# Performance work log

Hardware: AMD Instinct MI355X
Metric: run time of the kernel (lower is better)

The kernel has to match this reference:

```python
import jax, jax.numpy as jnp
import numpy as np

E, D, H = 8, 512, 2048  # num_experts, features, features*mlp_ratio
B, S = 4, 512


def _lecun(key, shape):
    fan_in = shape[-2] if len(shape) >= 2 else shape[0]
    return jax.random.normal(key, shape, dtype=jnp.float32) / jnp.sqrt(jnp.float32(fan_in))


def setup_inputs() -> dict:
    key = jax.random.key(0)
    ks = jax.random.split(key, 8)
    return {
        'x_real': jax.random.normal(ks[0], (B, S, D), dtype=jnp.float32),
        'x_imag': jax.random.normal(ks[1], (B, S, D), dtype=jnp.float32),
        # gating Dense over concat([amp, phase]) -> in_features = 2*D
        'gate_W': _lecun(ks[2], (2 * D, E)),
        'gate_b': jnp.zeros((E,), jnp.float32),
        # per-expert ComplexLinear 1: D -> H
        'W1r': _lecun(ks[3], (E, D, H)),
        'W1i': _lecun(ks[4], (E, D, H)),
        'b1r': jnp.zeros((E, H), jnp.float32),
        'b1i': jnp.zeros((E, H), jnp.float32),
        # per-expert ComplexModReLU bias
        'mod_b': jnp.zeros((E, H), jnp.float32),
        # per-expert ComplexLinear 2: H -> D
        'W2r': _lecun(ks[5], (E, H, D)),
        'W2i': _lecun(ks[6], (E, H, D)),
        'b2r': jnp.zeros((E, D), jnp.float32),
        'b2i': jnp.zeros((E, D), jnp.float32),
    }


def reference(x_real, x_imag, gate_W, gate_b, W1r, W1i, b1r, b1i, mod_b, W2r, W2i, b2r, b2i):
    eps = 1e-10
    # --- gating: scores over [|z|, angle(z)] ---
    amp = jnp.sqrt(x_real ** 2 + x_imag ** 2)            # |z|, [B,S,D]
    phase = jnp.arctan2(x_imag, x_real)                  # angle(z)
    routing_input = jnp.concatenate([amp, phase], axis=-1)  # [B,S,2D]
    scores = routing_input @ gate_W + gate_b             # [B,S,E]
    probs = jax.nn.softmax(scores, axis=-1)
    idx = jnp.argmax(probs, axis=-1)                     # [B,S] top-1 expert

    # --- all experts dense (faithful to reference): complex linear 1 ---
    # (Wr + iWi)(xr + ixi) : hr = xr Wr - xi Wi ; hi = xr Wi + xi Wr
    h_r = (jnp.einsum('bsd,edh->ebsh', x_real, W1r)
           - jnp.einsum('bsd,edh->ebsh', x_imag, W1i)) + b1r[:, None, None, :]
    h_i = (jnp.einsum('bsd,edh->ebsh', x_real, W1i)
           + jnp.einsum('bsd,edh->ebsh', x_imag, W1r)) + b1i[:, None, None, :]

    # --- ComplexModReLU: relu(|z|+b) * z / (|z|+eps), |z| = sqrt(r^2+i^2+eps) ---
    a = jnp.sqrt(h_r ** 2 + h_i ** 2 + eps)              # [E,B,S,H]
    scale = jax.nn.relu(a + mod_b[:, None, None, :]) / (a + eps)
    h_r = h_r * scale
    h_i = h_i * scale

    # --- complex linear 2 ---
    o_r = (jnp.einsum('ebsh,ehd->ebsd', h_r, W2r)
           - jnp.einsum('ebsh,ehd->ebsd', h_i, W2i)) + b2r[:, None, None, :]
    o_i = (jnp.einsum('ebsh,ehd->ebsd', h_r, W2i)
           + jnp.einsum('ebsh,ehd->ebsd', h_i, W2r)) + b2i[:, None, None, :]

    # --- mask + weight (top-1): out = sum_e out_e * probs[...,e] * (argmax==e) ---
    e_ids = jnp.arange(probs.shape[-1])
    w = jnp.transpose(probs, (2, 0, 1)) * (idx[None, :, :] == e_ids[:, None, None])  # [E,B,S]
    out_r = jnp.einsum('ebs,ebsd->bsd', w, o_r)
    out_i = jnp.einsum('ebs,ebsd->bsd', w, o_i)
    return (out_r, out_i)
```

## Files before the change

### kernel.cpp

```cpp
#include <hip/hip_runtime.h>
#include <math.h>

#define NE 8
#define ND 512
#define NH 2048
#define NT 2048

typedef __attribute__((ext_vector_type(8))) short short8;
typedef __attribute__((ext_vector_type(4))) float f32x4;

#define GLL(g, d) __builtin_amdgcn_global_load_lds( \
    (const __attribute__((address_space(1))) void*)(g), \
    (__attribute__((address_space(3))) void*)(d), 16, 0, 0)

__device__ __forceinline__ unsigned short f2bf(float x) {
    unsigned int u = __builtin_bit_cast(unsigned int, x);
    u += 0x7FFFu + ((u >> 16) & 1u);
    return (unsigned short)(u >> 16);
}

__device__ __forceinline__ short8 neg8(short8 v) {
    int4 u = __builtin_bit_cast(int4, v);
    u.x ^= 0x80008000; u.y ^= 0x80008000; u.z ^= 0x80008000; u.w ^= 0x80008000;
    return __builtin_bit_cast(short8, u);
}

__device__ __forceinline__ short8 lds8(const unsigned short* p) {
    return *(const short8*)p;
}

__global__ __launch_bounds__(256) void gate_kernel(
    const float* __restrict__ xr, const float* __restrict__ xi,
    const float* __restrict__ gW, const float* __restrict__ gb,
    float* __restrict__ gate_w,
    int* __restrict__ counts, int* __restrict__ tok_list)
{
    int t = blockIdx.x;
    int tid = threadIdx.x;
    const float* xrt = xr + (size_t)t * ND;
    const float* xit = xi + (size_t)t * ND;

    float acc[NE] = {0,0,0,0,0,0,0,0};
    for (int r = tid; r < 2 * ND; r += 256) {
        int d = r & (ND - 1);
        float a = xrt[d], b = xit[d];
        float v = (r < ND) ? sqrtf(a * a + b * b) : atan2f(b, a);
        const float4* g = (const float4*)(gW + (size_t)r * NE);
        float4 g0 = g[0], g1 = g[1];
        acc[0] += v * g0.x; acc[1] += v * g0.y; acc[2] += v * g0.z; acc[3] += v * g0.w;
        acc[4] += v * g1.x; acc[5] += v * g1.y; acc[6] += v * g1.z; acc[7] += v * g1.w;
    }
    #pragma unroll
    for (int e = 0; e < NE; e++) {
        for (int off = 32; off > 0; off >>= 1)
            acc[e] += __shfl_down(acc[e], off, 64);
    }
    __shared__ float part[4][NE];
    int wave = tid >> 6, lane = tid & 63;
    if (lane == 0) {
        #pragma unroll
        for (int e = 0; e < NE; e++) part[wave][e] = acc[e];
    }
    __syncthreads();
    if (tid == 0) {
        float s[NE];
        #pragma unroll
        for (int e = 0; e < NE; e++)
            s[e] = part[0][e] + part[1][e] + part[2][e] + part[3][e] + gb[e];
        int amax = 0; float m = s[0];
        #pragma unroll
        for (int e = 1; e < NE; e++) if (s[e] > m) { m = s[e]; amax = e; }
        float denom = 0.f;
        #pragma unroll
        for (int e = 0; e < NE; e++) denom += expf(s[e] - m);
        gate_w[t] = 1.0f / denom;
        int pos = atomicAdd(&counts[amax], 1);
        tok_list[amax * NT + pos] = t;
    }
}

__global__ __launch_bounds__(256) void convx_kernel(
    const float* __restrict__ xr, const float* __restrict__ xi,
    unsigned short* __restrict__ obr, unsigned short* __restrict__ obi)
{
    int i = blockIdx.x * 256 + threadIdx.x;
    float4 vr = ((const float4*)xr)[i];
    float4 vi = ((const float4*)xi)[i];
    ((ushort4*)obr)[i] = make_ushort4(f2bf(vr.x), f2bf(vr.y), f2bf(vr.z), f2bf(vr.w));
    ((ushort4*)obi)[i] = make_ushort4(f2bf(vi.x), f2bf(vi.y), f2bf(vi.z), f2bf(vi.w));
}

__global__ __launch_bounds__(256) void transw_kernel(
    const float* __restrict__ s0, unsigned short* __restrict__ d0,
    const float* __restrict__ s1, unsigned short* __restrict__ d1,
    int R, int C)
{
    __shared__ float tile[64][65];
    int e = blockIdx.z;
    int c0 = blockIdx.x * 64, r0 = blockIdx.y * 64;
    size_t off = (size_t)e * R * C;
    int tid = threadIdx.x;
    #pragma unroll
    for (int p = 0; p < 2; ++p) {
        const float* src = (p ? s1 : s0) + off;
        unsigned short* dst = (p ? d1 : d0) + off;
        if (p) __syncthreads();
        for (int i = 0; i < 16; ++i) {
            int idx = tid + i * 256;
            int r = idx >> 6, c = idx & 63;
            tile[r][c] = src[(size_t)(r0 + r) * C + c0 + c];
        }
        __syncthreads();
        for (int i = 0; i < 16; ++i) {
            int idx = tid + i * 256;
            int c = idx >> 6, r = idx & 63;
            dst[(size_t)(c0 + c) * R + r0 + r] = f2bf(tile[r][c]);
        }
    }
}

__global__ __launch_bounds__(256, 4) void moe1_kernel(
    const unsigned short* __restrict__ xbr, const unsigned short* __restrict__ xbi,
    const unsigned short* __restrict__ w1tr, const unsigned short* __restrict__ w1ti,
    const float* __restrict__ b1r, const float* __restrict__ b1i,
    const float* __restrict__ mod_b,
    const int* __restrict__ counts, const int* __restrict__ tok_list,
    unsigned short* __restrict__ hr, unsigned short* __restrict__ hi)
{
    int e = blockIdx.z;
    int n = counts[e];
    int mbase = blockIdx.y * 64;
    if (mbase >= n) return;
    int n0 = blockIdx.x * 64;
    int tid = threadIdx.x;
    int w = tid >> 6, l = tid & 63;
    int l15 = l & 15, quad = l >> 4;

    __shared__ unsigned short sAr[64 * 64];
    __shared__ unsigned short sAi[64 * 64];
    __shared__ unsigned short sBr[64 * 64];
    __shared__ unsigned short sBi[64 * 64];
    __shared__ int toks[64];

    const int* tl = tok_list + e * NT;
    if (tid < 64) {
        int idx = mbase + tid;
        toks[tid] = tl[idx < n ? idx : n - 1];
    }
    __syncthreads();

    int swz = (((l & 7) ^ ((l >> 3) & 7)) * 8);
    int ra0 = toks[w * 16 + (l >> 3)];
    int ra1 = toks[w * 16 + 8 + (l >> 3)];
    const unsigned short* gAr0 = xbr + (size_t)ra0 * ND + swz;
    const unsigned short* gAi0 = xbi + (size_t)ra0 * ND + swz;
    const unsigned short* gAr1 = xbr + (size_t)ra1 * ND + swz;
    const unsigned short* gAi1 = xbi + (size_t)ra1 * ND + swz;
    size_t brow = (size_t)e * NH + n0 + w * 16 + (l >> 3);
    const unsigned short* gBr0 = w1tr + brow * ND + swz;
    const unsigned short* gBr1 = w1tr + (brow + 8) * ND + swz;
    const unsigned short* gBi0 = w1ti + brow * ND + swz;
    const unsigned short* gBi1 = w1ti + (brow + 8) * ND + swz;

    unsigned short* dAr0 = sAr + (w * 16) * 64;
    unsigned short* dAr1 = sAr + (w * 16 + 8) * 64;
    unsigned short* dAi0 = sAi + (w * 16) * 64;
    unsigned short* dAi1 = sAi + (w * 16 + 8) * 64;
    unsigned short* dBr0 = sBr + (w * 16) * 64;
    unsigned short* dBr1 = sBr + (w * 16 + 8) * 64;
    unsigned short* dBi0 = sBi + (w * 16) * 64;
    unsigned short* dBi1 = sBi + (w * 16 + 8) * 64;

    f32x4 accr[4] = {}, acci[4] = {};

    for (int kt = 0; kt < ND / 64; ++kt) {
        __syncthreads();
        int ko = kt * 64;
        GLL(gAr0 + ko, dAr0); GLL(gAi0 + ko, dAi0);
        GLL(gAr1 + ko, dAr1); GLL(gAi1 + ko, dAi1);
        GLL(gBr0 + ko, dBr0); GLL(gBr1 + ko, dBr1);
        GLL(gBi0 + ko, dBi0); GLL(gBi1 + ko, dBi1);
        __syncthreads();
        #pragma unroll
        for (int ks = 0; ks < 2; ++ks) {
            int pa = ((ks * 4 + quad) ^ (l15 & 7)) * 8;
            short8 br  = lds8(sBr + (w * 16 + l15) * 64 + pa);
            short8 bi2 = lds8(sBi + (w * 16 + l15) * 64 + pa);
            #pragma unroll
            for (int m = 0; m < 4; ++m) {
                short8 ar  = lds8(sAr + (m * 16 + l15) * 64 + pa);
                short8 ai2 = lds8(sAi + (m * 16 + l15) * 64 + pa);
                short8 an  = neg8(ai2);
                accr[m] = __builtin_amdgcn_mfma_f32_16x16x32_bf16(ar,  br,  accr[m], 0, 0, 0);
                accr[m] = __builtin_amdgcn_mfma_f32_16x16x32_bf16(an,  bi2, accr[m], 0, 0, 0);
                acci[m] = __builtin_amdgcn_mfma_f32_16x16x32_bf16(ar,  bi2, acci[m], 0, 0, 0);
                acci[m] = __builtin_amdgcn_mfma_f32_16x16x32_bf16(ai2, br,  acci[m], 0, 0, 0);
            }
        }
    }

    int col = n0 + w * 16 + l15;
    float bre = b1r[(size_t)e * NH + col];
    float bie = b1i[(size_t)e * NH + col];
    float mbv = mod_b[(size_t)e * NH + col];
    #pragma unroll
    for (int m = 0; m < 4; ++m) {
        #pragma unroll
        for (int r = 0; r < 4; ++r) {
            int tix = m * 16 + quad * 4 + r;
            if (mbase + tix >= n) continue;
            int tok = toks[tix];
            float vr = accr[m][r] + bre;
            float vi = acci[m][r] + bie;
            float a = sqrtf(vr * vr + vi * vi + 1e-10f);
            float sc = fmaxf(a + mbv, 0.0f) / (a + 1e-10f);
            hr[(size_t)tok * NH + col] = f2bf(vr * sc);
            hi[(size_t)tok * NH + col] = f2bf(vi * sc);
        }
    }
}

__global__ __launch_bounds__(256, 4) void moe2_kernel(
    const unsigned short* __restrict__ hr, const unsigned short* __restrict__ hi,
    const unsigned short* __restrict__ w2tr, const unsigned short* __restrict__ w2ti,
    const float* __restrict__ b2r, const float* __restrict__ b2i,
    const int* __restrict__ counts, const int* __restrict__ tok_list,
    const float* __restrict__ gate_w,
    float* __restrict__ out)
{
    int e = blockIdx.z >> 2;
    int ksl = blockIdx.z & 3;
    int n = counts[e];
    int mbase = blockIdx.y * 64;
    if (mbase >= n) return;
    int n0 = blockIdx.x * 64;
    int kbase = ksl * (NH / 4);
    int tid = threadIdx.x;
    int w = tid >> 6, l = tid & 63;
    int l15 = l & 15, quad = l >> 4;

    __shared__ unsigned short sAr[64 * 64];
    __shared__ unsigned short sAi[64 * 64];
    __shared__ unsigned short sBr[64 * 64];
    __shared__ unsigned short sBi[64 * 64];
    __shared__ int toks[64];

    const int* tl = tok_list + e * NT;
    if (tid < 64) {
        int idx = mbase + tid;
        toks[tid] = tl[idx < n ? idx : n - 1];
    }
    __syncthreads();

    int swz = (((l & 7) ^ ((l >> 3) & 7)) * 8);
    int ra0 = toks[w * 16 + (l >> 3)];
    int ra1 = toks[w * 16 + 8 + (l >> 3)];
    const unsigned short* gAr0 = hr + (size_t)ra0 * NH + kbase + swz;
    const unsigned short* gAi0 = hi + (size_t)ra0 * NH + kbase + swz;
    const unsigned short* gAr1 = hr + (size_t)ra1 * NH + kbase + swz;
    const unsigned short* gAi1 = hi + (size_t)ra1 * NH + kbase + swz;
    size_t brow = (size_t)e * ND + n0 + w * 16 + (l >> 3);
    const unsigned short* gBr0 = w2tr + brow * NH + kbase + swz;
    const unsigned short* gBr1 = w2tr + (brow + 8) * NH + kbase + swz;
    const unsigned short* gBi0 = w2ti + brow * NH + kbase + swz;
    const unsigned short* gBi1 = w2ti + (brow + 8) * NH + kbase + swz;

    unsigned short* dAr0 = sAr + (w * 16) * 64;
    unsigned short* dAr1 = sAr + (w * 16 + 8) * 64;
    unsigned short* dAi0 = sAi + (w * 16) * 64;
    unsigned short* dAi1 = sAi + (w * 16 + 8) * 64;
    unsigned short* dBr0 = sBr + (w * 16) * 64;
    unsigned short* dBr1 = sBr + (w * 16 + 8) * 64;
    unsigned short* dBi0 = sBi + (w * 16) * 64;
    unsigned short* dBi1 = sBi + (w * 16 + 8) * 64;

    f32x4 accr[4] = {}, acci[4] = {};

    for (int kt = 0; kt < (NH / 4) / 64; ++kt) {
        __syncthreads();
        int ko = kt * 64;
        GLL(gAr0 + ko, dAr0); GLL(gAi0 + ko, dAi0);
        GLL(gAr1 + ko, dAr1); GLL(gAi1 + ko, dAi1);
        GLL(gBr0 + ko, dBr0); GLL(gBr1 + ko, dBr1);
        GLL(gBi0 + ko, dBi0); GLL(gBi1 + ko, dBi1);
        __syncthreads();
        #pragma unroll
        for (int ks = 0; ks < 2; ++ks) {
            int pa = ((ks * 4 + quad) ^ (l15 & 7)) * 8;
            short8 br  = lds8(sBr + (w * 16 + l15) * 64 + pa);
            short8 bi2 = lds8(sBi + (w * 16 + l15) * 64 + pa);
            #pragma unroll
            for (int m = 0; m < 4; ++m) {
                short8 ar  = lds8(sAr + (m * 16 + l15) * 64 + pa);
                short8 ai2 = lds8(sAi + (m * 16 + l15) * 64 + pa);
                short8 an  = neg8(ai2);
                accr[m] = __builtin_amdgcn_mfma_f32_16x16x32_bf16(ar,  br,  accr[m], 0, 0, 0);
                accr[m] = __builtin_amdgcn_mfma_f32_16x16x32_bf16(an,  bi2, accr[m], 0, 0, 0);
                acci[m] = __builtin_amdgcn_mfma_f32_16x16x32_bf16(ar,  bi2, acci[m], 0, 0, 0);
                acci[m] = __builtin_amdgcn_mfma_f32_16x16x32_bf16(ai2, br,  acci[m], 0, 0, 0);
            }
        }
    }

    int col = n0 + w * 16 + l15;
    float bre = (ksl == 0) ? b2r[(size_t)e * ND + col] : 0.0f;
    float bie = (ksl == 0) ? b2i[(size_t)e * ND + col] : 0.0f;
    #pragma unroll
    for (int m = 0; m < 4; ++m) {
        #pragma unroll
        for (int r = 0; r < 4; ++r) {
            int tix = m * 16 + quad * 4 + r;
            if (mbase + tix >= n) continue;
            int tok = toks[tix];
            float gw = gate_w[tok];
            atomicAdd(&out[(size_t)tok * ND + col], (accr[m][r] + bre) * gw);
            atomicAdd(&out[(size_t)NT * ND + (size_t)tok * ND + col], (acci[m][r] + bie) * gw);
        }
    }
}

extern "C" void kernel_launch(void* const* d_in, const int* in_sizes, int n_in,
                              void* d_out, int out_size, void* d_ws, size_t ws_size,
                              hipStream_t stream) {
    const float* xr   = (const float*)d_in[0];
    const float* xi   = (const float*)d_in[1];
    const float* gW   = (const float*)d_in[2];
    const float* gb   = (const float*)d_in[3];
    const float* W1r  = (const float*)d_in[4];
    const float* W1i  = (const float*)d_in[5];
    const float* b1r  = (const float*)d_in[6];
    const float* b1i  = (const float*)d_in[7];
    const float* modb = (const float*)d_in[8];
    const float* W2r  = (const float*)d_in[9];
    const float* W2i  = (const float*)d_in[10];
    const float* b2r  = (const float*)d_in[11];
    const float* b2i  = (const float*)d_in[12];
    float* out = (float*)d_out;

    char* ws = (char*)d_ws;
    int*   counts   = (int*)ws;
    float* gate_w   = (float*)(ws + 256);
    int*   tok_list = (int*)(ws + 256 + 8192);
    size_t off = 256 + 8192 + (size_t)NE * NT * 4;
    unsigned short* xbr  = (unsigned short*)(ws + off); off += (size_t)NT * ND * 2;
    unsigned short* xbi  = (unsigned short*)(ws + off); off += (size_t)NT * ND * 2;
    unsigned short* w1tr = (unsigned short*)(ws + off); off += (size_t)NE * ND * NH * 2;
    unsigned short* w1ti = (unsigned short*)(ws + off); off += (size_t)NE * ND * NH * 2;
    unsigned short* w2tr = (unsigned short*)(ws + off); off += (size_t)NE * ND * NH * 2;
    unsigned short* w2ti = (unsigned short*)(ws + off); off += (size_t)NE * ND * NH * 2;
    unsigned short* h_r  = (unsigned short*)(ws + off); off += (size_t)NT * NH * 2;
    unsigned short* h_i  = (unsigned short*)(ws + off); off += (size_t)NT * NH * 2;

    hipMemsetAsync(counts, 0, 64 * sizeof(int), stream);
    hipMemsetAsync(out, 0, (size_t)out_size * sizeof(float), stream);
    gate_kernel<<<NT, 256, 0, stream>>>(xr, xi, gW, gb, gate_w, counts, tok_list);
    convx_kernel<<<(NT * ND / 4) / 256, 256, 0, stream>>>(xr, xi, xbr, xbi);
    transw_kernel<<<dim3(NH / 64, ND / 64, NE), 256, 0, stream>>>(W1r, w1tr, W1i, w1ti, ND, NH);
    transw_kernel<<<dim3(ND / 64, NH / 64, NE), 256, 0, stream>>>(W2r, w2tr, W2i, w2ti, NH, ND);
    moe1_kernel<<<dim3(NH / 64, NT / 64, NE), 256, 0, stream>>>(
        xbr, xbi, w1tr, w1ti, b1r, b1i, modb, counts, tok_list, h_r, h_i);
    moe2_kernel<<<dim3(ND / 64, NT / 64, NE * 4), 256, 0, stream>>>(
        h_r, h_i, w2tr, w2ti, b2r, b2i, counts, tok_list, gate_w, out);
}
```

Measured before the change: 314.1 us.

## Double-buffer LDS tiles with K=32 steps in both expert GEMM kernels

Both grouped GEMM kernels now split the K-tile from 64 to 32 and double-buffer the A and B tiles in shared memory. The next tile's global-to-LDS loads are issued before computing on the current one, with explicit vmcnt waits and raw s_barrier instead of paired __syncthreads. The aim is to overlap global load latency with MFMA work. The swizzle is simplified to a 4-chunk XOR pattern, and halving K per stage doubles the number of barriers per tile.

```diff
diff --git a/kernel.cpp b/kernel.cpp
--- a/kernel.cpp
+++ b/kernel.cpp
@@ -12,6 +12,9 @@
 #define GLL(g, d) __builtin_amdgcn_global_load_lds( \
     (const __attribute__((address_space(1))) void*)(g), \
     (__attribute__((address_space(3))) void*)(d), 16, 0, 0)
+
+#define WAITCNT_VM4  0x0F74
+#define WAITCNT_VM0  0x0F70
 
 __device__ __forceinline__ unsigned short f2bf(float x) {
     unsigned int u = __builtin_bit_cast(unsigned int, x);
@@ -136,10 +139,10 @@
     int w = tid >> 6, l = tid & 63;
     int l15 = l & 15, quad = l >> 4;
 
-    __shared__ unsigned short sAr[64 * 64];
-    __shared__ unsigned short sAi[64 * 64];
-    __shared__ unsigned short sBr[64 * 64];
-    __shared__ unsigned short sBi[64 * 64];
+    __shared__ unsigned short sAr[2][64 * 32];
+    __shared__ unsigned short sAi[2][64 * 32];
+    __shared__ unsigned short sBr[2][64 * 32];
+    __shared__ unsigned short sBi[2][64 * 32];
     __shared__ int toks[64];
 
     const int* tl = tok_list + e * NT;
@@ -149,47 +152,44 @@
     }
     __syncthreads();
 
-    int swz = (((l & 7) ^ ((l >> 3) & 7)) * 8);
-    int ra0 = toks[w * 16 + (l >> 3)];
-    int ra1 = toks[w * 16 + 8 + (l >> 3)];
-    const unsigned short* gAr0 = xbr + (size_t)ra0 * ND + swz;
-    const unsigned short* gAi0 = xbi + (size_t)ra0 * ND + swz;
-    const unsigned short* gAr1 = xbr + (size_t)ra1 * ND + swz;
-    const unsigned short* gAi1 = xbi + (size_t)ra1 * ND + swz;
-    size_t brow = (size_t)e * NH + n0 + w * 16 + (l >> 3);
-    const unsigned short* gBr0 = w1tr + brow * ND + swz;
-    const unsigned short* gBr1 = w1tr + (brow + 8) * ND + swz;
-    const unsigned short* gBi0 = w1ti + brow * ND + swz;
-    const unsigned short* gBi1 = w1ti + (brow + 8) * ND + swz;
-
-    unsigned short* dAr0 = sAr + (w * 16) * 64;
-    unsigned short* dAr1 = sAr + (w * 16 + 8) * 64;
-    unsigned short* dAi0 = sAi + (w * 16) * 64;
-    unsigned short* dAi1 = sAi + (w * 16 + 8) * 64;
-    unsigned short* dBr0 = sBr + (w * 16) * 64;
-    unsigned short* dBr1 = sBr + (w * 16 + 8) * 64;
-    unsigned short* dBi0 = sBi + (w * 16) * 64;
-    unsigned short* dBi1 = sBi + (w * 16 + 8) * 64;
+    int r = tid >> 2;
+    int pc = tid & 3;
+    int gc = pc ^ ((r >> 1) & 3);
+    int tokA = toks[r];
+    const unsigned short* gAr = xbr + (size_t)tokA * ND + gc * 8;
+    const unsigned short* gAi = xbi + (size_t)tokA * ND + gc * 8;
+    size_t browB = (size_t)e * NH + n0 + r;
+    const unsigned short* gBr = w1tr + browB * ND + gc * 8;
+    const unsigned short* gBi = w1ti + browB * ND + gc * 8;
+    int woff = w * 512;
+
+    int perm8 = ((quad ^ (l15 >> 1)) & 3) * 8;
+    int browF = (w * 16 + l15) * 32 + perm8;
+    int arow0 = l15 * 32 + perm8;
 
     f32x4 accr[4] = {}, acci[4] = {};
 
-    for (int kt = 0; kt < ND / 64; ++kt) {
-        __syncthreads();
-        int ko = kt * 64;
-        GLL(gAr0 + ko, dAr0); GLL(gAi0 + ko, dAi0);
-        GLL(gAr1 + ko, dAr1); GLL(gAi1 + ko, dAi1);
-        GLL(gBr0 + ko, dBr0); GLL(gBr1 + ko, dBr1);
-        GLL(gBi0 + ko, dBi0); GLL(gBi1 + ko, dBi1);
-        __syncthreads();
-        #pragma unroll
-        for (int ks = 0; ks < 2; ++ks) {
-            int pa = ((ks * 4 + quad) ^ (l15 & 7)) * 8;
-            short8 br  = lds8(sBr + (w * 16 + l15) * 64 + pa);
-            short8 bi2 = lds8(sBi + (w * 16 + l15) * 64 + pa);
+    GLL(gAr, &sAr[0][woff]); GLL(gAi, &sAi[0][woff]);
+    GLL(gBr, &sBr[0][woff]); GLL(gBi, &sBi[0][woff]);
+
+    int cur = 0;
+    const int NKT = ND / 32;
+    #pragma unroll 2
+    for (int kt = 0; kt < NKT - 1; ++kt) {
+        int nxt = cur ^ 1;
+        int ko = (kt + 1) * 32;
+        GLL(gAr + ko, &sAr[nxt][woff]); GLL(gAi + ko, &sAi[nxt][woff]);
+        GLL(gBr + ko, &sBr[nxt][woff]); GLL(gBi + ko, &sBi[nxt][woff]);
+        __builtin_amdgcn_s_waitcnt(WAITCNT_VM4);
+        __builtin_amdgcn_s_barrier();
+        __builtin_amdgcn_sched_barrier(0);
+        {
+            short8 br  = lds8(&sBr[cur][browF]);
+            short8 bi2 = lds8(&sBi[cur][browF]);
             #pragma unroll
             for (int m = 0; m < 4; ++m) {
-                short8 ar  = lds8(sAr + (m * 16 + l15) * 64 + pa);
-                short8 ai2 = lds8(sAi + (m * 16 + l15) * 64 + pa);
+                short8 ar  = lds8(&sAr[cur][arow0 + m * 512]);
+                short8 ai2 = lds8(&sAi[cur][arow0 + m * 512]);
                 short8 an  = neg8(ai2);
                 accr[m] = __builtin_amdgcn_mfma_f32_16x16x32_bf16(ar,  br,  accr[m], 0, 0, 0);
                 accr[m] = __builtin_amdgcn_mfma_f32_16x16x32_bf16(an,  bi2, accr[m], 0, 0, 0);
@@ -197,6 +197,26 @@
                 acci[m] = __builtin_amdgcn_mfma_f32_16x16x32_bf16(ai2, br,  acci[m], 0, 0, 0);
             }
         }
+        __builtin_amdgcn_sched_barrier(0);
+        __builtin_amdgcn_s_barrier();
+        cur = nxt;
+    }
+    __builtin_amdgcn_s_waitcnt(WAITCNT_VM0);
+    __builtin_amdgcn_s_barrier();
+    __builtin_amdgcn_sched_barrier(0);
+    {
+        short8 br  = lds8(&sBr[cur][browF]);
+        short8 bi2 = lds8(&sBi[cur][browF]);
+        #pragma unroll
+        for (int m = 0; m < 4; ++m) {
+            short8 ar  = lds8(&sAr[cur][arow0 + m * 512]);
+            short8 ai2 = lds8(&sAi[cur][arow0 + m * 512]);
+            short8 an  = neg8(ai2);
+            accr[m] = __builtin_amdgcn_mfma_f32_16x16x32_bf16(ar,  br,  accr[m], 0, 0, 0);
+            accr[m] = __builtin_amdgcn_mfma_f32_16x16x32_bf16(an,  bi2, accr[m], 0, 0, 0);
+            acci[m] = __builtin_amdgcn_mfma_f32_16x16x32_bf16(ar,  bi2, acci[m], 0, 0, 0);
+            acci[m] = __builtin_amdgcn_mfma_f32_16x16x32_bf16(ai2, br,  acci[m], 0, 0, 0);
+        }
     }
 
     int col = n0 + w * 16 + l15;
@@ -206,12 +226,12 @@
     #pragma unroll
     for (int m = 0; m < 4; ++m) {
         #pragma unroll
-        for (int r = 0; r < 4; ++r) {
-            int tix = m * 16 + quad * 4 + r;
+        for (int rr = 0; rr < 4; ++rr) {
+            int tix = m * 16 + quad * 4 + rr;
             if (mbase + tix >= n) continue;
             int tok = toks[tix];
-            float vr = accr[m][r] + bre;
-            float vi = acci[m][r] + bie;
+            float vr = accr[m][rr] + bre;
+            float vi = acci[m][rr] + bie;
             float a = sqrtf(vr * vr + vi * vi + 1e-10f);
             float sc = fmaxf(a + mbv, 0.0f) / (a + 1e-10f);
             hr[(size_t)tok * NH + col] = f2bf(vr * sc);
@@ -239,10 +259,10 @@
     int w = tid >> 6, l = tid & 63;
     int l15 = l & 15, quad = l >> 4;
 
-    __shared__ unsigned short sAr[64 * 64];
-    __shared__ unsigned short sAi[64 * 64];
-    __shared__ unsigned short sBr[64 * 64];
-    __shared__ unsigned short sBi[64 * 64];
+    __shared__ unsigned short sAr[2][64 * 32];
+    __shared__ unsigned short sAi[2][64 * 32];
+    __shared__ unsigned short sBr[2][64 * 32];
+    __shared__ unsigned short sBi[2][64 * 32];
     __shared__ int toks[64];
 
     const int* tl = tok_list + e * NT;
@@ -252,47 +272,44 @@
     }
     __syncthreads();
 
-    int swz = (((l & 7) ^ ((l >> 3) & 7)) * 8);
-    int ra0 = toks[w * 16 + (l >> 3)];
-    int ra1 = toks[w * 16 + 8 + (l >> 3)];
-    const unsigned short* gAr0 = hr + (size_t)ra0 * NH + kbase + swz;
-    const unsigned short* gAi0 = hi + (size_t)ra0 * NH + kbase + swz;
-    const unsigned short* gAr1 = hr + (size_t)ra1 * NH + kbase + swz;
-    const unsigned short* gAi1 = hi + (size_t)ra1 * NH + kbase + swz;
-    size_t brow = (size_t)e * ND + n0 + w * 16 + (l >> 3);
-    const unsigned short* gBr0 = w2tr + brow * NH + kbase + swz;
-    const unsigned short* gBr1 = w2tr + (brow + 8) * NH + kbase + swz;
-    const unsigned short* gBi0 = w2ti + brow * NH + kbase + swz;
-    const unsigned short* gBi1 = w2ti + (brow + 8) * NH + kbase + swz;
-
-    unsigned short* dAr0 = sAr + (w * 16) * 64;
-    unsigned short* dAr1 = sAr + (w * 16 + 8) * 64;
-    unsigned short* dAi0 = sAi + (w * 16) * 64;
-    unsigned short* dAi1 = sAi + (w * 16 + 8) * 64;
-    unsigned short* dBr0 = sBr + (w * 16) * 64;
-    unsigned short* dBr1 = sBr + (w * 16 + 8) * 64;
-    unsigned short* dBi0 = sBi + (w * 16) * 64;
-    unsigned short* dBi1 = sBi + (w * 16 + 8) * 64;
+    int r = tid >> 2;
+    int pc = tid & 3;
+    int gc = pc ^ ((r >> 1) & 3);
+    int tokA = toks[r];
+    const unsigned short* gAr = hr + (size_t)tokA * NH + kbase + gc * 8;
+    const unsigned short* gAi = hi + (size_t)tokA * NH + kbase + gc * 8;
+    size_t browB = (size_t)e * ND + n0 + r;
+    const unsigned short* gBr = w2tr + browB * NH + kbase + gc * 8;
+    const unsigned short* gBi = w2ti + browB * NH + kbase + gc * 8;
+    int woff = w * 512;
+
+    int perm8 = ((quad ^ (l15 >> 1)) & 3) * 8;
+    int browF = (w * 16 + l15) * 32 + perm8;
+    int arow0 = l15 * 32 + perm8;
 
     f32x4 accr[4] = {}, acci[4] = {};
 
-    for (int kt = 0; kt < (NH / 4) / 64; ++kt) {
-        __syncthreads();
-        int ko = kt * 64;
-        GLL(gAr0 + ko, dAr0); GLL(gAi0 + ko, dAi0);
-        GLL(gAr1 + ko, dAr1); GLL(gAi1 + ko, dAi1);
-        GLL(gBr0 + ko, dBr0); GLL(gBr1 + ko, dBr1);
-        GLL(gBi0 + ko, dBi0); GLL(gBi1 + ko, dBi1);
-        __syncthreads();
-        #pragma unroll
-        for (int ks = 0; ks < 2; ++ks) {
-            int pa = ((ks * 4 + quad) ^ (l15 & 7)) * 8;
-            short8 br  = lds8(sBr + (w * 16 + l15) * 64 + pa);
-            short8 bi2 = lds8(sBi + (w * 16 + l15) * 64 + pa);
+    GLL(gAr, &sAr[0][woff]); GLL(gAi, &sAi[0][woff]);
+    GLL(gBr, &sBr[0][woff]); GLL(gBi, &sBi[0][woff]);
+
+    int cur = 0;
+    const int NKT = (NH / 4) / 32;
+    #pragma unroll 2
+    for (int kt = 0; kt < NKT - 1; ++kt) {
+        int nxt = cur ^ 1;
+        int ko = (kt + 1) * 32;
+        GLL(gAr + ko, &sAr[nxt][woff]); GLL(gAi + ko, &sAi[nxt][woff]);
+        GLL(gBr + ko, &sBr[nxt][woff]); GLL(gBi + ko, &sBi[nxt][woff]);
+        __builtin_amdgcn_s_waitcnt(WAITCNT_VM4);
+        __builtin_amdgcn_s_barrier();
+        __builtin_amdgcn_sched_barrier(0);
+        {
+            short8 br  = lds8(&sBr[cur][browF]);
+            short8 bi2 = lds8(&sBi[cur][browF]);
             #pragma unroll
             for (int m = 0; m < 4; ++m) {
-                short8 ar  = lds8(sAr + (m * 16 + l15) * 64 + pa);
-                short8 ai2 = lds8(sAi + (m * 16 + l15) * 64 + pa);
+                short8 ar  = lds8(&sAr[cur][arow0 + m * 512]);
+                short8 ai2 = lds8(&sAi[cur][arow0 + m * 512]);
                 short8 an  = neg8(ai2);
                 accr[m] = __builtin_amdgcn_mfma_f32_16x16x32_bf16(ar,  br,  accr[m], 0, 0, 0);
                 accr[m] = __builtin_amdgcn_mfma_f32_16x16x32_bf16(an,  bi2, accr[m], 0, 0, 0);
@@ -300,6 +317,26 @@
                 acci[m] = __builtin_amdgcn_mfma_f32_16x16x32_bf16(ai2, br,  acci[m], 0, 0, 0);
             }
         }
+        __builtin_amdgcn_sched_barrier(0);
+        __builtin_amdgcn_s_barrier();
+        cur = nxt;
+    }
+    __builtin_amdgcn_s_waitcnt(WAITCNT_VM0);
+    __builtin_amdgcn_s_barrier();
+    __builtin_amdgcn_sched_barrier(0);
+    {
+        short8 br  = lds8(&sBr[cur][browF]);
+        short8 bi2 = lds8(&sBi[cur][browF]);
+        #pragma unroll
+        for (int m = 0; m < 4; ++m) {
+            short8 ar  = lds8(&sAr[cur][arow0 + m * 512]);
+            short8 ai2 = lds8(&sAi[cur][arow0 + m * 512]);
+            short8 an  = neg8(ai2);
+            accr[m] = __builtin_amdgcn_mfma_f32_16x16x32_bf16(ar,  br,  accr[m], 0, 0, 0);
+            accr[m] = __builtin_amdgcn_mfma_f32_16x16x32_bf16(an,  bi2, accr[m], 0, 0, 0);
+            acci[m] = __builtin_amdgcn_mfma_f32_16x16x32_bf16(ar,  bi2, acci[m], 0, 0, 0);
+            acci[m] = __builtin_amdgcn_mfma_f32_16x16x32_bf16(ai2, br,  acci[m], 0, 0, 0);
+        }
     }
 
     int col = n0 + w * 16 + l15;
@@ -308,13 +345,13 @@
     #pragma unroll
     for (int m = 0; m < 4; ++m) {
         #pragma unroll
-        for (int r = 0; r < 4; ++r) {
-            int tix = m * 16 + quad * 4 + r;
+        for (int rr = 0; rr < 4; ++rr) {
+            int tix = m * 16 + quad * 4 + rr;
             if (mbase + tix >= n) continue;
             int tok = toks[tix];
             float gw = gate_w[tok];
-            atomicAdd(&out[(size_t)tok * ND + col], (accr[m][r] + bre) * gw);
-            atomicAdd(&out[(size_t)NT * ND + (size_t)tok * ND + col], (acci[m][r] + bie) * gw);
+            atomicAdd(&out[(size_t)tok * ND + col], (accr[m][rr] + bre) * gw);
+            atomicAdd(&out[(size_t)NT * ND + (size_t)tok * ND + col], (acci[m][rr] + bie) * gw);
         }
     }
 }
```

Result: slower. 324.3 us (+3.2%).
